# Kernel optimization log

Hardware: AMD Instinct MI355X
Metric: run time of the kernel (lower is better)

Reference implementation:

```python
import jax, jax.numpy as jnp
import numpy as np

C, H, W = 96, 128, 128
D_EMB, D_HID = 2, 16


def setup_inputs() -> dict:
    key = jax.random.key(0)
    k1, k2, k3, k4, k5 = jax.random.split(key, 5)
    x = jax.random.normal(k1, (16, C, H, W), dtype=jnp.float32)
    # MLP params: Linear(d_emb, d_hidden) -> ReLU -> Linear(d_hidden, hidden_size)
    W1 = jax.random.normal(k2, (D_EMB, D_HID), dtype=jnp.float32) / np.sqrt(D_EMB)
    b1 = jax.random.normal(k3, (D_HID,), dtype=jnp.float32) * 0.01
    W2 = jax.random.normal(k4, (D_HID, C), dtype=jnp.float32) / np.sqrt(D_HID)
    b2 = jax.random.normal(k5, (C,), dtype=jnp.float32) * 0.01
    return {"x": x, "W1": W1, "b1": b1, "W2": W2, "b2": b2}


def reference(x, W1, b1, W2, b2):
    B, Cc, Hh, Ww = x.shape
    # positional grid (y/H, x/W) in [0,1], shape [H, W, 2]
    gy, gx = jnp.meshgrid(jnp.linspace(0.0, 1.0, Hh), jnp.linspace(0.0, 1.0, Ww), indexing="ij")
    pe = jnp.stack([gy, gx], axis=-1).reshape(-1, 2)  # [H*W, 2]
    hid = jax.nn.relu(pe @ W1 + b1)                   # [H*W, d_hidden]
    k = (hid @ W2 + b2).T.reshape(Cc, Hh, Ww)         # [C, H, W]
    fh, fw = 2 * Hh, 2 * Ww
    k_f = jnp.fft.rfft2(k, s=(fh, fw))                # [C, fh, fw//2+1]
    x_f = jnp.fft.rfft2(x, s=(fh, fw))                # [B, C, fh, fw//2+1]
    # torch: rfft2 norm='backward' (unscaled) + irfft2 norm='forward' (unscaled)
    # => net factor of fh*fw, replicated faithfully via norm='forward'.
    y = jnp.fft.irfft2(x_f * k_f[None], s=(fh, fw), norm="forward")
    y = y[..., :Hh, :Ww]
    return y + x  # residual=True, gelu=False
```

## Files before the change

### kernel.cpp

```cpp
#include <hip/hip_runtime.h>
#include <hip/hip_fp16.h>

#define TWO_PI 6.283185307179586f
#define PI_F   3.14159265358979f

#define HH 128
#define WW 128
#define FN 256
#define NF 129
#define CC 96
#define BB 16

#define SCL_DN 0.0009765625f
#define SCL_UP 1024.0f

typedef unsigned int uint2v __attribute__((ext_vector_type(2)));

__device__ __forceinline__ float2 cmul(float2 a, float2 b){
  return make_float2(a.x*b.x - a.y*b.y, a.x*b.y + a.y*b.x);
}
__device__ __forceinline__ float2 cmulc(float2 a, float2 b){
  return make_float2(a.x*b.x + a.y*b.y, a.x*b.y - a.y*b.x);
}
__device__ __forceinline__ float2 cadd(float2 a, float2 b){ return make_float2(a.x+b.x, a.y+b.y); }
__device__ __forceinline__ float2 csub(float2 a, float2 b){ return make_float2(a.x-b.x, a.y-b.y); }
__device__ __forceinline__ float2 shflx(float2 v, int m){
  float2 r; r.x = __shfl_xor(v.x, m, 64); r.y = __shfl_xor(v.y, m, 64); return r;
}
__device__ __forceinline__ float2 shfli(float2 v, int idx){
  float2 r; r.x = __shfl(v.x, idx, 64); r.y = __shfl(v.y, idx, 64); return r;
}
__device__ __forceinline__ unsigned short f2h(float v){ return __half_as_ushort(__float2half(v)); }
__device__ __forceinline__ float h2f(unsigned short u){ return __half2float(__ushort_as_half(u)); }

__device__ __forceinline__ void swp32(float2 v, float2& lo, float2& hi){
  uint2v rx = __builtin_amdgcn_permlane32_swap(__float_as_uint(v.x), __float_as_uint(v.x), false, false);
  uint2v ry = __builtin_amdgcn_permlane32_swap(__float_as_uint(v.y), __float_as_uint(v.y), false, false);
  lo = make_float2(__uint_as_float(rx[0]), __uint_as_float(ry[0]));
  hi = make_float2(__uint_as_float(rx[1]), __uint_as_float(ry[1]));
}
__device__ __forceinline__ void swp16(float2 v, float2& lo, float2& hi){
  uint2v rx = __builtin_amdgcn_permlane16_swap(__float_as_uint(v.x), __float_as_uint(v.x), false, false);
  uint2v ry = __builtin_amdgcn_permlane16_swap(__float_as_uint(v.y), __float_as_uint(v.y), false, false);
  lo = make_float2(__uint_as_float(rx[0]), __uint_as_float(ry[0]));
  hi = make_float2(__uint_as_float(rx[1]), __uint_as_float(ry[1]));
}
template<int CTRL>
__device__ __forceinline__ float2 dppx(float2 v){
  float2 r;
  r.x = __uint_as_float((unsigned)__builtin_amdgcn_update_dpp(0, (int)__float_as_uint(v.x), CTRL, 0xF, 0xF, true));
  r.y = __uint_as_float((unsigned)__builtin_amdgcn_update_dpp(0, (int)__float_as_uint(v.y), CTRL, 0xF, 0xF, true));
  return r;
}
#define DPP_XOR1 0xB1
#define DPP_XOR2 0x4E

struct Tw {
  float2 w128a, w128b, w64;
  float2 wc[5];
  float2 wf[5];
  float  sg[5];
  float  sg1;
};

__device__ __forceinline__ void tw_init(Tw& t, int l){
  float s, c;
  sincosf(-TWO_PI * (float)l * (1.0f/256.0f), &s, &c);
  t.w128a = make_float2(c, s);
  t.w128b = make_float2(s, -c);
  t.w64   = make_float2(c*c - s*s, 2.0f*c*s);
  const int hs[5] = {32,16,8,4,2};
#pragma unroll
  for (int i = 0; i < 5; ++i){
    int h = hs[i];
    float ang = -PI_F * (float)(l & (h-1)) / (float)h;
    sincosf(ang, &s, &c);
    t.wc[i] = make_float2(c, s);
    bool dn = (l & h) != 0;
    t.wf[i] = dn ? t.wc[i] : make_float2(1.0f, 0.0f);
    t.sg[i] = dn ? -1.0f : 1.0f;
  }
  t.sg1 = (l & 1) ? -1.0f : 1.0f;
}

#define FX_OTHER(X, OTHER, SG, WF) { \
  float2 o_ = OTHER; float2 s_; \
  s_.x = fmaf(SG, X.x, o_.x); s_.y = fmaf(SG, X.y, o_.y); \
  X = cmul(WF, s_); }
#define FX_LOHI(X, SWPF, SG, WF) { \
  float2 lo_, hi_, s_; SWPF(X, lo_, hi_); \
  s_.x = fmaf(SG, hi_.x, lo_.x); s_.y = fmaf(SG, hi_.y, lo_.y); \
  X = cmul(WF, s_); }
#define IX_LOHI(X, SWPF, SG, WC) { \
  float2 lo_, hi_, m_; SWPF(X, lo_, hi_); \
  m_ = cmulc(WC, hi_); \
  X.x = fmaf(SG, m_.x, lo_.x); X.y = fmaf(SG, m_.y, lo_.y); }
#define IX_OTHER(X, OTHER, UP, SG, WC) { \
  float2 o_ = OTHER; \
  float2 A_ = UP ? X : o_; \
  float2 B_ = UP ? o_ : X; \
  float2 m_ = cmulc(WC, B_); \
  X.x = fmaf(SG, m_.x, A_.x); X.y = fmaf(SG, m_.y, A_.y); }

__device__ __forceinline__ void fft256_fwd_padded(float2& x0, float2& x1,
                                                  float2& x2, float2& x3,
                                                  const Tw& t, int l){
  x2 = cmul(x0, t.w128a);
  x3 = cmul(x1, t.w128b);
  float2 a = x0, b = x1;
  x0 = cadd(a, b); x1 = cmul(csub(a, b), t.w64);
  a = x2; b = x3;
  x2 = cadd(a, b); x3 = cmul(csub(a, b), t.w64);
  FX_LOHI(x0, swp32, t.sg[0], t.wf[0]);
  FX_LOHI(x1, swp32, t.sg[0], t.wf[0]);
  FX_LOHI(x2, swp32, t.sg[0], t.wf[0]);
  FX_LOHI(x3, swp32, t.sg[0], t.wf[0]);
  FX_LOHI(x0, swp16, t.sg[1], t.wf[1]);
  FX_LOHI(x1, swp16, t.sg[1], t.wf[1]);
  FX_LOHI(x2, swp16, t.sg[1], t.wf[1]);
  FX_LOHI(x3, swp16, t.sg[1], t.wf[1]);
  FX_OTHER(x0, shflx(x0, 8), t.sg[2], t.wf[2]);
  FX_OTHER(x1, shflx(x1, 8), t.sg[2], t.wf[2]);
  FX_OTHER(x2, shflx(x2, 8), t.sg[2], t.wf[2]);
  FX_OTHER(x3, shflx(x3, 8), t.sg[2], t.wf[2]);
  FX_OTHER(x0, shflx(x0, 4), t.sg[3], t.wf[3]);
  FX_OTHER(x1, shflx(x1, 4), t.sg[3], t.wf[3]);
  FX_OTHER(x2, shflx(x2, 4), t.sg[3], t.wf[3]);
  FX_OTHER(x3, shflx(x3, 4), t.sg[3], t.wf[3]);
  FX_OTHER(x0, dppx<DPP_XOR2>(x0), t.sg[4], t.wf[4]);
  FX_OTHER(x1, dppx<DPP_XOR2>(x1), t.sg[4], t.wf[4]);
  FX_OTHER(x2, dppx<DPP_XOR2>(x2), t.sg[4], t.wf[4]);
  FX_OTHER(x3, dppx<DPP_XOR2>(x3), t.sg[4], t.wf[4]);
  {
    float2 o;
    o = dppx<DPP_XOR1>(x0); x0.x = fmaf(t.sg1, x0.x, o.x); x0.y = fmaf(t.sg1, x0.y, o.y);
    o = dppx<DPP_XOR1>(x1); x1.x = fmaf(t.sg1, x1.x, o.x); x1.y = fmaf(t.sg1, x1.y, o.y);
    o = dppx<DPP_XOR1>(x2); x2.x = fmaf(t.sg1, x2.x, o.x); x2.y = fmaf(t.sg1, x2.y, o.y);
    o = dppx<DPP_XOR1>(x3); x3.x = fmaf(t.sg1, x3.x, o.x); x3.y = fmaf(t.sg1, x3.y, o.y);
  }
}

__device__ __forceinline__ void fft256_inv_crop(float2& x0, float2& x1,
                                                float2& x2, float2& x3,
                                                const Tw& t, int l){
  {
    float2 o;
    o = dppx<DPP_XOR1>(x0); x0.x = fmaf(t.sg1, x0.x, o.x); x0.y = fmaf(t.sg1, x0.y, o.y);
    o = dppx<DPP_XOR1>(x1); x1.x = fmaf(t.sg1, x1.x, o.x); x1.y = fmaf(t.sg1, x1.y, o.y);
    o = dppx<DPP_XOR1>(x2); x2.x = fmaf(t.sg1, x2.x, o.x); x2.y = fmaf(t.sg1, x2.y, o.y);
    o = dppx<DPP_XOR1>(x3); x3.x = fmaf(t.sg1, x3.x, o.x); x3.y = fmaf(t.sg1, x3.y, o.y);
  }
  {
    bool up = (l & 2) == 0;
    IX_OTHER(x0, dppx<DPP_XOR2>(x0), up, t.sg[4], t.wc[4]);
    IX_OTHER(x1, dppx<DPP_XOR2>(x1), up, t.sg[4], t.wc[4]);
    IX_OTHER(x2, dppx<DPP_XOR2>(x2), up, t.sg[4], t.wc[4]);
    IX_OTHER(x3, dppx<DPP_XOR2>(x3), up, t.sg[4], t.wc[4]);
  }
  {
    bool up = (l & 4) == 0;
    IX_OTHER(x0, shflx(x0, 4), up, t.sg[3], t.wc[3]);
    IX_OTHER(x1, shflx(x1, 4), up, t.sg[3], t.wc[3]);
    IX_OTHER(x2, shflx(x2, 4), up, t.sg[3], t.wc[3]);
    IX_OTHER(x3, shflx(x3, 4), up, t.sg[3], t.wc[3]);
  }
  {
    bool up = (l & 8) == 0;
    IX_OTHER(x0, shflx(x0, 8), up, t.sg[2], t.wc[2]);
    IX_OTHER(x1, shflx(x1, 8), up, t.sg[2], t.wc[2]);
    IX_OTHER(x2, shflx(x2, 8), up, t.sg[2], t.wc[2]);
    IX_OTHER(x3, shflx(x3, 8), up, t.sg[2], t.wc[2]);
  }
  IX_LOHI(x0, swp16, t.sg[1], t.wc[1]);
  IX_LOHI(x1, swp16, t.sg[1], t.wc[1]);
  IX_LOHI(x2, swp16, t.sg[1], t.wc[1]);
  IX_LOHI(x3, swp16, t.sg[1], t.wc[1]);
  IX_LOHI(x0, swp32, t.sg[0], t.wc[0]);
  IX_LOHI(x1, swp32, t.sg[0], t.wc[0]);
  IX_LOHI(x2, swp32, t.sg[0], t.wc[0]);
  IX_LOHI(x3, swp32, t.sg[0], t.wc[0]);
  {
    float2 w = make_float2(t.w64.x, -t.w64.y);
    float2 t0 = cmul(w, x1); x1 = csub(x0, t0); x0 = cadd(x0, t0);
    float2 t1 = cmul(w, x3); x3 = csub(x2, t1); x2 = cadd(x2, t1);
  }
  {
    float2 wa = make_float2(t.w128a.x, -t.w128a.y);
    float2 wb = make_float2(t.w128b.x, -t.w128b.y);
    x0 = cadd(x0, cmul(wa, x2));
    x1 = cadd(x1, cmul(wb, x3));
  }
}


__global__ __launch_bounds__(512) void kprep_col(const float* __restrict__ W1,
                                                 const float* __restrict__ b1,
                                                 const float* __restrict__ W2,
                                                 const float* __restrict__ b2,
                                                 float2* __restrict__ Khat){
  __shared__ float sRe[NF*65];
  __shared__ float sIm[NF*65];
  const int S = 65;
  int t = threadIdx.x, l = t & 63, w = t >> 6;
  int c  = blockIdx.x >> 1;
  int q0B = (blockIdx.x & 1) * 64;
  Tw tw; tw_init(tw, l);
  int r6 = __brev((unsigned)l) >> 26;
  int l63 = l ^ 63;
  int p0 = __brev((unsigned)((64 - r6) & 63)) >> 26;

  float w1y[16], w1x[16], bb1[16], w2r[16];
#pragma unroll
  for (int h = 0; h < 16; ++h){
    w1y[h] = W1[h]; w1x[h] = W1[16+h]; bb1[h] = b1[h];
    w2r[h] = W2[h*CC + c] * 0.25f;
  }
  float bb2 = b2[c] * 0.25f;
  float gy0 = (float)l        * (1.0f/127.0f);
  float gy1 = (float)(l + 64) * (1.0f/127.0f);

#define SEPST32(Z, P, ROW) { \
  sRe[(ROW)*S + qa] = Z.x + P.x; sIm[(ROW)*S + qa] = Z.y - P.y; \
  sRe[(ROW)*S + qb] = Z.y + P.y; sIm[(ROW)*S + qb] = P.x - Z.x; }

  for (int ji = 0; ji < 4; ++ji){
    int jj = w*4 + ji;
    int qa = 2*jj, qb = 2*jj + 1;
    float gxa = (float)(q0B + qa) * (1.0f/127.0f);
    float gxb = (float)(q0B + qb) * (1.0f/127.0f);
    float a0 = bb2, a1 = bb2, bq0 = bb2, bq1 = bb2;
#pragma unroll
    for (int h = 0; h < 16; ++h){
      float hxa = gxa*w1x[h] + bb1[h];
      float hxb = gxb*w1x[h] + bb1[h];
      a0  += fmaxf(gy0*w1y[h] + hxa, 0.0f) * w2r[h];
      a1  += fmaxf(gy1*w1y[h] + hxa, 0.0f) * w2r[h];
      bq0 += fmaxf(gy0*w1y[h] + hxb, 0.0f) * w2r[h];
      bq1 += fmaxf(gy1*w1y[h] + hxb, 0.0f) * w2r[h];
    }
    float2 x0 = make_float2(a0, bq0);
    float2 x1 = make_float2(a1, bq1);
    float2 x2, x3;
    fft256_fwd_padded(x0, x1, x2, x3, tw, l);
    float2 f0p = shfli(x0, p0);
    float2 f2p = shfli(x3, l63);
    float2 f1p = shfli(x1, l63);
    float2 f3p = shfli(x2, l63);
    if (r6 <= 32){ SEPST32(x0, f0p, 4*r6); }
    if (r6 <= 31){
      SEPST32(x2, f2p, 4*r6+1);
      SEPST32(x1, f1p, 4*r6+2);
      SEPST32(x3, f3p, 4*r6+3);
    }
  }
#undef SEPST32
  __syncthreads();
  for (int idx = t; idx < NF*64; idx += 512){
    int u = idx >> 6, qq = idx & 63;
    Khat[((size_t)c*NF + u)*FN + q0B + qq] = make_float2(sRe[u*S+qq], sIm[u*S+qq]);
  }
}

__global__ __launch_bounds__(512) void kprep_row(float2* __restrict__ Khat){
  int t = threadIdx.x, l = t & 63, w = t >> 6;
  int c = blockIdx.x >> 2, part = blockIdx.x & 3;
  Tw tw; tw_init(tw, l);
  for (int j = w; ; j += 8){
    int u = part + 4*j;
    if (u >= NF) break;
    float2* kp = Khat + ((size_t)c*NF + u)*FN;
    float2 x0 = kp[l], x1 = kp[64 + l], x2, x3;
    fft256_fwd_padded(x0, x1, x2, x3, tw, l);
    kp[l] = x0; kp[64 + l] = x1; kp[128 + l] = x2; kp[192 + l] = x3;
  }
}

__global__ __launch_bounds__(512) void fused_conv(const float* __restrict__ x,
                                                  const float2* __restrict__ Khat,
                                                  float* __restrict__ out){
  __shared__ unsigned short hRe[131*130];
  __shared__ unsigned short hIm[131*130];
  const int S = 130;
  int t = threadIdx.x, l = t & 63, w = t >> 6;
  int blk = blockIdx.x;
  int c = blk >> 4, b = blk & 15;
  const float* xp = x   + ((size_t)b*CC + c)*(HH*WW);
  float*       yp = out + ((size_t)b*CC + c)*(HH*WW);
  Tw tw; tw_init(tw, l);
  int r6 = __brev((unsigned)l) >> 26;
  int l63 = l ^ 63;
  int p0 = __brev((unsigned)((64 - r6) & 63)) >> 26;

  for (int i = t; i < HH*WW; i += 512){
    int p = i >> 7, q = i & 127;
    unsigned int ub = __float_as_uint(xp[i]);
    hRe[p*S + q] = (unsigned short)(ub >> 16);
    hIm[p*S + q] = (unsigned short)(ub & 0xffffu);
  }
  __syncthreads();
#define SEPST16(Z, P, ROW) { \
  float ax_ = Z.x + P.x, ay_ = Z.y - P.y; \
  float bx_ = Z.y + P.y, by_ = P.x - Z.x; \
  *(ushort2*)&hRe[(ROW)*S + q0] = make_ushort2(f2h(ax_), f2h(bx_)); \
  *(ushort2*)&hIm[(ROW)*S + q0] = make_ushort2(f2h(ay_), f2h(by_)); }

  for (int ji = 0; ji < 8; ++ji){
    int jj = w*8 + ji;
    int q0 = 2*jj;
    ushort2 hr0 = *(const ushort2*)&hRe[l*S + q0];
    ushort2 hi0 = *(const ushort2*)&hIm[l*S + q0];
    ushort2 hr1 = *(const ushort2*)&hRe[(l+64)*S + q0];
    ushort2 hi1 = *(const ushort2*)&hIm[(l+64)*S + q0];
    float2 x0 = make_float2(__uint_as_float(((unsigned)hr0.x << 16) | hi0.x),
                            __uint_as_float(((unsigned)hr0.y << 16) | hi0.y));
    float2 x1 = make_float2(__uint_as_float(((unsigned)hr1.x << 16) | hi1.x),
                            __uint_as_float(((unsigned)hr1.y << 16) | hi1.y));
    float2 x2, x3;
    fft256_fwd_padded(x0, x1, x2, x3, tw, l);
    float2 f0p = shfli(x0, p0);
    float2 f2p = shfli(x3, l63);
    float2 f1p = shfli(x1, l63);
    float2 f3p = shfli(x2, l63);
    if (r6 <= 32){ SEPST16(x0, f0p, r6); }
    if (r6 <= 31){
      SEPST16(x2, f2p, 33+r6);
      SEPST16(x1, f1p, 66+r6);
      SEPST16(x3, f3p, 99+r6);
    }
  }
#undef SEPST16
  __syncthreads();
  for (int u = w; u < NF; u += 8){
    int pr = (u >> 2) + 33*(u & 3);
    float2 x0 = make_float2(h2f(hRe[pr*S + l]),      h2f(hIm[pr*S + l]));
    float2 x1 = make_float2(h2f(hRe[pr*S + 64 + l]), h2f(hIm[pr*S + 64 + l]));
    float2 x2, x3;
    fft256_fwd_padded(x0, x1, x2, x3, tw, l);
    const float2* kp = Khat + ((size_t)c*NF + u)*FN;
    x0 = cmul(x0, kp[l]);
    x1 = cmul(x1, kp[64 + l]);
    x2 = cmul(x2, kp[128 + l]);
    x3 = cmul(x3, kp[192 + l]);
    fft256_inv_crop(x0, x1, x2, x3, tw, l);
    hRe[pr*S + l]      = f2h(x0.x * SCL_DN); hIm[pr*S + l]      = f2h(x0.y * SCL_DN);
    hRe[pr*S + 64 + l] = f2h(x1.x * SCL_DN); hIm[pr*S + 64 + l] = f2h(x1.y * SCL_DN);
  }
  __syncthreads();
#define GATHV(X, ROWA, ROWB, COND) { \
  int row_ = (COND) ? (ROWA) : (ROWB); \
  float s_ = (COND) ? -1.0f : 1.0f; \
  ushort2 hr_ = *(const ushort2*)&hRe[row_*S + q0]; \
  ushort2 hi_ = *(const ushort2*)&hIm[row_*S + q0]; \
  float re0_ = h2f(hr_.x), re1_ = h2f(hr_.y); \
  float im0_ = h2f(hi_.x), im1_ = h2f(hi_.y); \
  X = make_float2(fmaf(s_, im1_, re0_), fmaf(-s_, im0_, re1_)); }

  for (int ji = 0; ji < 8; ++ji){
    int jj = w*8 + ji;
    int q0 = 2*jj;
    float2 x0, x1, x2, x3;
    GATHV(x0, r6,    64-r6,  r6 <= 32);
    GATHV(x2, 33+r6, 162-r6, r6 <= 31);
    GATHV(x1, 66+r6, 129-r6, r6 <= 31);
    GATHV(x3, 99+r6, 96-r6,  r6 <= 31);
    fft256_inv_crop(x0, x1, x2, x3, tw, l);
    unsigned ua0 = __float_as_uint(x0.x * SCL_UP);
    unsigned ub0 = __float_as_uint(x0.y * SCL_UP);
    *(ushort2*)&hRe[l*S + q0] = make_ushort2((unsigned short)(ua0 >> 16), (unsigned short)(ub0 >> 16));
    *(ushort2*)&hIm[l*S + q0] = make_ushort2((unsigned short)(ua0 & 0xffffu), (unsigned short)(ub0 & 0xffffu));
    unsigned ua1 = __float_as_uint(x1.x * SCL_UP);
    unsigned ub1 = __float_as_uint(x1.y * SCL_UP);
    *(ushort2*)&hRe[(l+64)*S + q0] = make_ushort2((unsigned short)(ua1 >> 16), (unsigned short)(ub1 >> 16));
    *(ushort2*)&hIm[(l+64)*S + q0] = make_ushort2((unsigned short)(ua1 & 0xffffu), (unsigned short)(ub1 & 0xffffu));
  }
#undef GATHV
  __syncthreads();
  for (int i = t; i < HH*WW; i += 512){
    int p = i >> 7, q = i & 127;
    unsigned int ub = ((unsigned int)hRe[p*S + q] << 16) | hIm[p*S + q];
    yp[i] = __uint_as_float(ub) + xp[i];
  }
}

extern "C" void kernel_launch(void* const* d_in, const int* in_sizes, int n_in,
                              void* d_out, int out_size, void* d_ws, size_t ws_size,
                              hipStream_t stream) {
  const float* x  = (const float*)d_in[0];
  const float* W1 = (const float*)d_in[1];
  const float* b1 = (const float*)d_in[2];
  const float* W2 = (const float*)d_in[3];
  const float* b2 = (const float*)d_in[4];
  float* out = (float*)d_out;

  float2* Khat = (float2*)d_ws;

  kprep_col<<<CC*2, 512, 0, stream>>>(W1, b1, W2, b2, Khat);
  kprep_row<<<CC*4, 512, 0, stream>>>(Khat);
  fused_conv<<<CC*BB, 512, 0, stream>>>(x, Khat, out);
}
```

Baseline: 425.1 us.

## Pack shared spectrum as interleaved half2 words and merge DC/Nyquist column FFTs

Replaces the split hRe/hIm ushort shared arrays with one 32-bit array that holds either a full fp32 value or a packed half2 (re,im). Each shared access becomes a single dword or dwordx2 instead of two separate 16-bit accesses, and conversion uses the packed cvt_pkrtz instruction. The two purely real column spectra (u=0 and u=128) are handled as one complex FFT by warp 0, with the separation folded into the kernel multiply. This removes one FFT pair from the 129-row loop, so the loop runs a fixed 16 iterations per warp. The cost is extra branch divergence and more complex indexing for that special iteration, plus round-toward-zero rounding where the old code used round-to-nearest.

```diff
diff --git a/kernel.cpp b/kernel.cpp
--- a/kernel.cpp
+++ b/kernel.cpp
@@ -15,6 +15,7 @@
 #define SCL_UP 1024.0f
 
 typedef unsigned int uint2v __attribute__((ext_vector_type(2)));
+typedef __fp16 half2v __attribute__((ext_vector_type(2)));
 
 __device__ __forceinline__ float2 cmul(float2 a, float2 b){
   return make_float2(a.x*b.x - a.y*b.y, a.x*b.y + a.y*b.x);
@@ -32,6 +33,13 @@
 }
 __device__ __forceinline__ unsigned short f2h(float v){ return __half_as_ushort(__float2half(v)); }
 __device__ __forceinline__ float h2f(unsigned short u){ return __half2float(__ushort_as_half(u)); }
+__device__ __forceinline__ unsigned pkh2(float a, float b){
+  union { half2v h; unsigned u; } cv;
+  cv.h = __builtin_amdgcn_cvt_pkrtz(a, b);
+  return cv.u;
+}
+__device__ __forceinline__ float h2lo(unsigned u){ return h2f((unsigned short)(u & 0xffffu)); }
+__device__ __forceinline__ float h2hi(unsigned u){ return h2f((unsigned short)(u >> 16)); }
 
 __device__ __forceinline__ void swp32(float2 v, float2& lo, float2& hi){
   uint2v rx = __builtin_amdgcn_permlane32_swap(__float_as_uint(v.x), __float_as_uint(v.x), false, false);
@@ -278,8 +286,7 @@
 __global__ __launch_bounds__(512) void fused_conv(const float* __restrict__ x,
                                                   const float2* __restrict__ Khat,
                                                   float* __restrict__ out){
-  __shared__ unsigned short hRe[131*130];
-  __shared__ unsigned short hIm[131*130];
+  __shared__ unsigned int PL[131*130];
   const int S = 130;
   int t = threadIdx.x, l = t & 63, w = t >> 6;
   int blk = blockIdx.x;
@@ -293,28 +300,22 @@
 
   for (int i = t; i < HH*WW; i += 512){
     int p = i >> 7, q = i & 127;
-    unsigned int ub = __float_as_uint(xp[i]);
-    hRe[p*S + q] = (unsigned short)(ub >> 16);
-    hIm[p*S + q] = (unsigned short)(ub & 0xffffu);
+    PL[p*S + q] = __float_as_uint(xp[i]);
   }
   __syncthreads();
 #define SEPST16(Z, P, ROW) { \
-  float ax_ = Z.x + P.x, ay_ = Z.y - P.y; \
-  float bx_ = Z.y + P.y, by_ = P.x - Z.x; \
-  *(ushort2*)&hRe[(ROW)*S + q0] = make_ushort2(f2h(ax_), f2h(bx_)); \
-  *(ushort2*)&hIm[(ROW)*S + q0] = make_ushort2(f2h(ay_), f2h(by_)); }
+  uint2 st_; \
+  st_.x = pkh2(Z.x + P.x, Z.y - P.y); \
+  st_.y = pkh2(Z.y + P.y, P.x - Z.x); \
+  *(uint2*)&PL[(ROW)*S + q0] = st_; }
 
   for (int ji = 0; ji < 8; ++ji){
     int jj = w*8 + ji;
     int q0 = 2*jj;
-    ushort2 hr0 = *(const ushort2*)&hRe[l*S + q0];
-    ushort2 hi0 = *(const ushort2*)&hIm[l*S + q0];
-    ushort2 hr1 = *(const ushort2*)&hRe[(l+64)*S + q0];
-    ushort2 hi1 = *(const ushort2*)&hIm[(l+64)*S + q0];
-    float2 x0 = make_float2(__uint_as_float(((unsigned)hr0.x << 16) | hi0.x),
-                            __uint_as_float(((unsigned)hr0.y << 16) | hi0.y));
-    float2 x1 = make_float2(__uint_as_float(((unsigned)hr1.x << 16) | hi1.x),
-                            __uint_as_float(((unsigned)hr1.y << 16) | hi1.y));
+    uint2 v0 = *(const uint2*)&PL[l*S + q0];
+    uint2 v1 = *(const uint2*)&PL[(l+64)*S + q0];
+    float2 x0 = make_float2(__uint_as_float(v0.x), __uint_as_float(v0.y));
+    float2 x1 = make_float2(__uint_as_float(v1.x), __uint_as_float(v1.y));
     float2 x2, x3;
     fft256_fwd_padded(x0, x1, x2, x3, tw, l);
     float2 f0p = shfli(x0, p0);
@@ -330,30 +331,63 @@
   }
 #undef SEPST16
   __syncthreads();
-  for (int u = w; u < NF; u += 8){
-    int pr = (u >> 2) + 33*(u & 3);
-    float2 x0 = make_float2(h2f(hRe[pr*S + l]),      h2f(hIm[pr*S + l]));
-    float2 x1 = make_float2(h2f(hRe[pr*S + 64 + l]), h2f(hIm[pr*S + 64 + l]));
-    float2 x2, x3;
-    fft256_fwd_padded(x0, x1, x2, x3, tw, l);
-    const float2* kp = Khat + ((size_t)c*NF + u)*FN;
-    x0 = cmul(x0, kp[l]);
-    x1 = cmul(x1, kp[64 + l]);
-    x2 = cmul(x2, kp[128 + l]);
-    x3 = cmul(x3, kp[192 + l]);
-    fft256_inv_crop(x0, x1, x2, x3, tw, l);
-    hRe[pr*S + l]      = f2h(x0.x * SCL_DN); hIm[pr*S + l]      = f2h(x0.y * SCL_DN);
-    hRe[pr*S + 64 + l] = f2h(x1.x * SCL_DN); hIm[pr*S + 64 + l] = f2h(x1.y * SCL_DN);
+  for (int k = 0; k < 16; ++k){
+    int u = w + 8*k;
+    if (w == 0 && k == 0){
+      unsigned a0 = PL[l],           a1 = PL[64 + l];
+      unsigned c0 = PL[32*S + l],    c1 = PL[32*S + 64 + l];
+      float2 x0 = make_float2(h2lo(a0), h2lo(c0));
+      float2 x1 = make_float2(h2lo(a1), h2lo(c1));
+      float2 x2, x3;
+      fft256_fwd_padded(x0, x1, x2, x3, tw, l);
+      float2 f0p = shfli(x0, p0);
+      float2 f2p = shfli(x3, l63);
+      float2 f1p = shfli(x1, l63);
+      float2 f3p = shfli(x2, l63);
+      const float2* k0p = Khat + (size_t)c*NF*FN;
+      const float2* k1p = k0p + (size_t)128*FN;
+#define PKMUL(Z, P, OFF) { \
+      float2 A2_ = make_float2(Z.x + P.x, Z.y - P.y); \
+      float2 B2_ = make_float2(Z.y + P.y, P.x - Z.x); \
+      float2 m0_ = cmul(A2_, k0p[OFF]); \
+      float2 m1_ = cmul(B2_, k1p[OFF]); \
+      Z = make_float2(m0_.x - m1_.y, m0_.y + m1_.x); }
+      PKMUL(x0, f0p, l);
+      PKMUL(x2, f2p, 128 + l);
+      PKMUL(x1, f1p, 64 + l);
+      PKMUL(x3, f3p, 192 + l);
+#undef PKMUL
+      fft256_inv_crop(x0, x1, x2, x3, tw, l);
+      const float sc = SCL_DN * 0.5f;
+      PL[l]           = pkh2(x0.x * sc, 0.0f);
+      PL[32*S + l]    = pkh2(x0.y * sc, 0.0f);
+      PL[64 + l]      = pkh2(x1.x * sc, 0.0f);
+      PL[32*S + 64+l] = pkh2(x1.y * sc, 0.0f);
+    } else {
+      int pr = (u >> 2) + 33*(u & 3);
+      unsigned ua = PL[pr*S + l];
+      unsigned ub = PL[pr*S + 64 + l];
+      float2 x0 = make_float2(h2lo(ua), h2hi(ua));
+      float2 x1 = make_float2(h2lo(ub), h2hi(ub));
+      float2 x2, x3;
+      fft256_fwd_padded(x0, x1, x2, x3, tw, l);
+      const float2* kp = Khat + ((size_t)c*NF + u)*FN;
+      x0 = cmul(x0, kp[l]);
+      x1 = cmul(x1, kp[64 + l]);
+      x2 = cmul(x2, kp[128 + l]);
+      x3 = cmul(x3, kp[192 + l]);
+      fft256_inv_crop(x0, x1, x2, x3, tw, l);
+      PL[pr*S + l]      = pkh2(x0.x * SCL_DN, x0.y * SCL_DN);
+      PL[pr*S + 64 + l] = pkh2(x1.x * SCL_DN, x1.y * SCL_DN);
+    }
   }
   __syncthreads();
 #define GATHV(X, ROWA, ROWB, COND) { \
   int row_ = (COND) ? (ROWA) : (ROWB); \
   float s_ = (COND) ? -1.0f : 1.0f; \
-  ushort2 hr_ = *(const ushort2*)&hRe[row_*S + q0]; \
-  ushort2 hi_ = *(const ushort2*)&hIm[row_*S + q0]; \
-  float re0_ = h2f(hr_.x), re1_ = h2f(hr_.y); \
-  float im0_ = h2f(hi_.x), im1_ = h2f(hi_.y); \
-  X = make_float2(fmaf(s_, im1_, re0_), fmaf(-s_, im0_, re1_)); }
+  uint2 u_ = *(const uint2*)&PL[row_*S + q0]; \
+  X = make_float2(fmaf(s_, h2hi(u_.y), h2lo(u_.x)), \
+                  fmaf(-s_, h2hi(u_.x), h2lo(u_.y))); }
 
   for (int ji = 0; ji < 8; ++ji){
     int jj = w*8 + ji;
@@ -364,21 +398,19 @@
     GATHV(x1, 66+r6, 129-r6, r6 <= 31);
     GATHV(x3, 99+r6, 96-r6,  r6 <= 31);
     fft256_inv_crop(x0, x1, x2, x3, tw, l);
-    unsigned ua0 = __float_as_uint(x0.x * SCL_UP);
-    unsigned ub0 = __float_as_uint(x0.y * SCL_UP);
-    *(ushort2*)&hRe[l*S + q0] = make_ushort2((unsigned short)(ua0 >> 16), (unsigned short)(ub0 >> 16));
-    *(ushort2*)&hIm[l*S + q0] = make_ushort2((unsigned short)(ua0 & 0xffffu), (unsigned short)(ub0 & 0xffffu));
-    unsigned ua1 = __float_as_uint(x1.x * SCL_UP);
-    unsigned ub1 = __float_as_uint(x1.y * SCL_UP);
-    *(ushort2*)&hRe[(l+64)*S + q0] = make_ushort2((unsigned short)(ua1 >> 16), (unsigned short)(ub1 >> 16));
-    *(ushort2*)&hIm[(l+64)*S + q0] = make_ushort2((unsigned short)(ua1 & 0xffffu), (unsigned short)(ub1 & 0xffffu));
+    uint2 st0, st1;
+    st0.x = __float_as_uint(x0.x * SCL_UP);
+    st0.y = __float_as_uint(x0.y * SCL_UP);
+    *(uint2*)&PL[l*S + q0] = st0;
+    st1.x = __float_as_uint(x1.x * SCL_UP);
+    st1.y = __float_as_uint(x1.y * SCL_UP);
+    *(uint2*)&PL[(l+64)*S + q0] = st1;
   }
 #undef GATHV
   __syncthreads();
   for (int i = t; i < HH*WW; i += 512){
     int p = i >> 7, q = i & 127;
-    unsigned int ub = ((unsigned int)hRe[p*S + q] << 16) | hIm[p*S + q];
-    yp[i] = __uint_as_float(ub) + xp[i];
+    yp[i] = __uint_as_float(PL[p*S + q]) + xp[i];
   }
 }
 
```

Result: no change. 421.5 us (-0.9%).
